# Optimization experiments

Hardware: AMD Instinct MI355X
Metric: run time of the kernel (lower is better)

The kernel has to match this reference:

```python
import jax, jax.numpy as jnp
import numpy as np

B, T, I, H = 512, 256, 256, 512


def _lstm(x, Wih, Whh, bih, bhh):
    # x: [B, T, I]; Wih: [4H, I]; Whh: [4H, H]; gate order i, f, g, o (torch)
    Bv = x.shape[0]
    Hv = Whh.shape[1]
    xg = jnp.einsum('bti,gi->btg', x, Wih) + bih + bhh  # [B, T, 4H] (input projections hoisted out of scan)
    xg = jnp.transpose(xg, (1, 0, 2))  # [T, B, 4H]
    h0 = jnp.zeros((Bv, Hv), x.dtype)
    c0 = jnp.zeros((Bv, Hv), x.dtype)

    def step(carry, gx):
        h, c = carry
        g = gx + h @ Whh.T  # [B, 4H]
        i, f, gg, o = jnp.split(g, 4, axis=-1)
        i = jax.nn.sigmoid(i)
        f = jax.nn.sigmoid(f)
        gg = jnp.tanh(gg)
        o = jax.nn.sigmoid(o)
        c = f * c + i * gg
        h = o * jnp.tanh(c)
        return (h, c), h

    _, hs = jax.lax.scan(step, (h0, c0), xg)  # hs: [T, B, H]
    return jnp.transpose(hs, (1, 0, 2))  # [B, T, H]


def _bn1d(x, gamma, beta, eps=1e-5):
    # torch BatchNorm1d on [N, C, L] in training mode: per-channel stats over (N, L), biased var
    m = jnp.mean(x, axis=(0, 2), keepdims=True)
    v = jnp.var(x, axis=(0, 2), keepdims=True)
    return (x - m) * jax.lax.rsqrt(v + eps) * gamma[None, :, None] + beta[None, :, None]


def setup_inputs() -> dict:
    key = jax.random.key(0)
    ks = jax.random.split(key, 14)
    s = 1.0 / np.sqrt(H)
    return {
        'x': jax.random.normal(ks[0], (B, T, I), jnp.float32),
        'Wih': jax.random.uniform(ks[1], (4 * H, I), jnp.float32, -s, s),
        'Whh': jax.random.uniform(ks[2], (4 * H, H), jnp.float32, -s, s),
        'bih': jax.random.uniform(ks[3], (4 * H,), jnp.float32, -s, s),
        'bhh': jax.random.uniform(ks[4], (4 * H,), jnp.float32, -s, s),
        'fc1_w': jax.random.uniform(ks[5], (32, H), jnp.float32, -s, s),
        'fc1_b': jax.random.uniform(ks[6], (32,), jnp.float32, -s, s),
        'fc2_w': jax.random.uniform(ks[7], (1, 32), jnp.float32, -0.17, 0.17),
        'fc2_b': jax.random.uniform(ks[8], (1,), jnp.float32, -0.17, 0.17),
        'bn1_g': jnp.ones((T,), jnp.float32),
        'bn1_b': jnp.zeros((T,), jnp.float32),
        'bn2_g': jnp.ones((T,), jnp.float32),
        'bn2_b': jnp.zeros((T,), jnp.float32),
    }


def reference(x, Wih, Whh, bih, bhh, fc1_w, fc1_b, fc2_w, fc2_b, bn1_g, bn1_b, bn2_g, bn2_b):
    lstm_out = _lstm(x, Wih, Whh, bih, bhh)  # [B, T, H]
    a = jnp.einsum('bth,oh->bto', lstm_out, fc1_w) + fc1_b  # [B, T, 32]
    a = jax.nn.leaky_relu(_bn1d(a, bn1_g, bn1_b), negative_slope=0.1)
    z = jnp.einsum('bto,po->btp', a, fc2_w) + fc2_b  # [B, T, 1]
    out = jax.nn.relu(_bn1d(z, bn2_g, bn2_b))
    return out
```

## Files before the change

kernel.cpp:

```cpp
#include <hip/hip_runtime.h>

#define BB 512
#define TT 256
#define II 256
#define HH 512

typedef __attribute__((ext_vector_type(8))) short bf16x8;
typedef __attribute__((ext_vector_type(4))) float f32x4;

__device__ __forceinline__ unsigned short f2bf(float f) {
  union { float f; unsigned u; } v; v.f = f;
  unsigned r = v.u + 0x7fffu + ((v.u >> 16) & 1u);
  return (unsigned short)(r >> 16);
}

#define OFF_CNT   0
#define OFF_HSWZ  4096
#define OFF_XSWZ  1052672ULL
#define OFF_HIST  68161536ULL
#define ZERO_WORDS 263168

__global__ void zero_k(unsigned* __restrict__ p, int n) {
  int i = blockIdx.x * blockDim.x + threadIdx.x;
  if (i < n) p[i] = 0u;
}

__global__ __launch_bounds__(256) void prep_x(const float* __restrict__ x,
                                              unsigned char* __restrict__ ws) {
  __shared__ unsigned short xs[16][264];
  const int t = blockIdx.x >> 5, rc = blockIdx.x & 31;
  const int tid = threadIdx.x;
  {
    const int r = tid >> 4, seg = tid & 15;
    const float* src = x + ((size_t)(rc * 16 + r) * TT + t) * II + seg * 16;
    const float4* s4 = (const float4*)src;
#pragma unroll
    for (int q = 0; q < 4; ++q) {
      float4 v = s4[q];
      xs[r][seg * 16 + q * 4 + 0] = f2bf(v.x);
      xs[r][seg * 16 + q * 4 + 1] = f2bf(v.y);
      xs[r][seg * 16 + q * 4 + 2] = f2bf(v.z);
      xs[r][seg * 16 + q * 4 + 3] = f2bf(v.w);
    }
  }
  __syncthreads();
  const int lane = tid & 63;
  const int row16 = lane & 15, koff = (lane >> 4) * 8;
#pragma unroll
  for (int kc = tid >> 6; kc < 8; kc += 4) {
    union { unsigned short h[8]; uint4 v; } pk;
#pragma unroll
    for (int j = 0; j < 8; ++j) pk.h[j] = xs[row16][kc * 32 + koff + j];
    *(uint4*)(ws + OFF_XSWZ + (size_t)(t * 8 + kc) * 32768u +
              ((size_t)rc * 64 + lane) * 16) = pk.v;
  }
}

__global__ __launch_bounds__(512, 2) void lstm_persist(
    const float* __restrict__ Wih, const float* __restrict__ Whh,
    const float* __restrict__ bih, const float* __restrict__ bhh,
    unsigned char* __restrict__ ws)
{
  const int gid = blockIdx.x;
  const int group = gid & 7;
  const int m = gid >> 3;
  const int tid = threadIdx.x;
  const int wv = tid >> 6, lane = tid & 63;
  const int mb = wv & 3, kh = wv >> 2;
  const int lq = lane >> 4, ln = lane & 15;

  int* flags_g = (int*)(ws + OFF_CNT + (size_t)group * 512);
  unsigned char* xswz  = ws + OFF_XSWZ;
  unsigned char* hswz0 = ws + OFF_HSWZ;
  unsigned char* hswz1 = ws + OFF_HSWZ + 524288;
  unsigned char* hist  = ws + OFF_HIST;

  __shared__ int step_flag;
  if (tid == 0) step_flag = 0;

  bf16x8 Wf[12][4];
#pragma unroll
  for (int kk = 0; kk < 12; ++kk) {
    const int kb = (kh * 12 + kk) * 32 + lq * 8;
#pragma unroll
    for (int nt = 0; nt < 4; ++nt) {
      const int gcol = nt * 512 + m * 16 + ln;
      const float* s = (kb < 256) ? (Wih + (size_t)gcol * 256 + kb)
                                  : (Whh + (size_t)gcol * 512 + (kb - 256));
      bf16x8 w;
#pragma unroll
      for (int j = 0; j < 8; ++j) w[j] = (short)f2bf(s[j]);
      Wf[kk][nt] = w;
    }
  }

  float bia[4];
#pragma unroll
  for (int nt = 0; nt < 4; ++nt) {
    int gcol = nt * 512 + m * 16 + ln;
    bia[nt] = bih[gcol] + bhh[gcol];
  }

  __shared__ float g_s[64 * 68];
  __shared__ float h_s[64 * 17];

  const size_t aoff = ((size_t)(group * 4 + mb) * 64 + lane) * 16;
  float creg[4] = {0.f, 0.f, 0.f, 0.f};
  const f32x4 zero4 = {0.f, 0.f, 0.f, 0.f};

#pragma unroll 1
  for (int t = 0; t < 256; ++t) {
    unsigned char* hrd = (t & 1) ? hswz1 : hswz0;
    unsigned char* hwr = (t & 1) ? hswz0 : hswz1;

    f32x4 acc[4] = {zero4, zero4, zero4, zero4};

    if (kh == 0) {
#pragma unroll
      for (int kk = 0; kk < 8; ++kk) {
        bf16x8 a = *(const bf16x8*)(xswz + (size_t)(t * 8 + kk) * 32768u + aoff);
#pragma unroll
        for (int nt = 0; nt < 4; ++nt)
          acc[nt] = __builtin_amdgcn_mfma_f32_16x16x32_bf16(a, Wf[kk][nt], acc[nt], 0, 0, 0);
      }
    }

    if (t > 0) {
      if (wv == 4) {
        int iter = 0;
        for (;;) {
          int v = __hip_atomic_load(flags_g + (lane & 31), __ATOMIC_RELAXED,
                                    __HIP_MEMORY_SCOPE_AGENT);
          if (__all(v >= t)) break;
          if (++iter >= (1 << 17)) break;
          __builtin_amdgcn_s_sleep(1);
        }
        __hip_atomic_store(&step_flag, t, __ATOMIC_RELAXED,
                           __HIP_MEMORY_SCOPE_WORKGROUP);
      } else {
        int iter = 0;
        while (__hip_atomic_load(&step_flag, __ATOMIC_RELAXED,
                                 __HIP_MEMORY_SCOPE_WORKGROUP) < t
               && iter < (1 << 20)) {
          ++iter;
          __builtin_amdgcn_s_sleep(1);
        }
      }
      asm volatile("" ::: "memory");
    }

    if (kh == 0) {
      unsigned long long u0[4], u1[4];
#pragma unroll
      for (int p = 0; p < 4; ++p) {
        const unsigned long long* q =
            (const unsigned long long*)(hrd + (size_t)p * 32768u + aoff);
        u0[p] = __hip_atomic_load(q + 0, __ATOMIC_RELAXED, __HIP_MEMORY_SCOPE_AGENT);
        u1[p] = __hip_atomic_load(q + 1, __ATOMIC_RELAXED, __HIP_MEMORY_SCOPE_AGENT);
      }
#pragma unroll
      for (int kk = 0; kk < 4; ++kk) {
        union { unsigned long long q[2]; bf16x8 v; } u;
        u.q[0] = u0[kk]; u.q[1] = u1[kk];
#pragma unroll
        for (int nt = 0; nt < 4; ++nt)
          acc[nt] = __builtin_amdgcn_mfma_f32_16x16x32_bf16(u.v, Wf[8 + kk][nt], acc[nt], 0, 0, 0);
      }
    } else {
      unsigned long long u0[6], u1[6];
#pragma unroll
      for (int p = 0; p < 6; ++p) {
        const unsigned long long* q =
            (const unsigned long long*)(hrd + (size_t)(4 + p) * 32768u + aoff);
        u0[p] = __hip_atomic_load(q + 0, __ATOMIC_RELAXED, __HIP_MEMORY_SCOPE_AGENT);
        u1[p] = __hip_atomic_load(q + 1, __ATOMIC_RELAXED, __HIP_MEMORY_SCOPE_AGENT);
      }
#pragma unroll
      for (int kk = 0; kk < 12; ++kk) {
        const int slot = kk % 6;
        union { unsigned long long q[2]; bf16x8 v; } u;
        u.q[0] = u0[slot]; u.q[1] = u1[slot];
        if (kk < 6) {
          const unsigned long long* q =
              (const unsigned long long*)(hrd + (size_t)(10 + kk) * 32768u + aoff);
          u0[slot] = __hip_atomic_load(q + 0, __ATOMIC_RELAXED, __HIP_MEMORY_SCOPE_AGENT);
          u1[slot] = __hip_atomic_load(q + 1, __ATOMIC_RELAXED, __HIP_MEMORY_SCOPE_AGENT);
        }
#pragma unroll
        for (int nt = 0; nt < 4; ++nt)
          acc[nt] = __builtin_amdgcn_mfma_f32_16x16x32_bf16(u.v, Wf[kk][nt], acc[nt], 0, 0, 0);
      }
#pragma unroll
      for (int nt = 0; nt < 4; ++nt)
#pragma unroll
        for (int r = 0; r < 4; ++r)
          g_s[(mb * 16 + lq * 4 + r) * 68 + nt * 16 + ln] = acc[nt][r];
    }
    __syncthreads();

    if (kh == 0) {
#pragma unroll
      for (int r = 0; r < 4; ++r) {
        const int rw = mb * 16 + lq * 4 + r;
        float gi = acc[0][r] + g_s[rw * 68 + ln]      + bia[0];
        float gf = acc[1][r] + g_s[rw * 68 + 16 + ln] + bia[1];
        float gg = acc[2][r] + g_s[rw * 68 + 32 + ln] + bia[2];
        float go = acc[3][r] + g_s[rw * 68 + 48 + ln] + bia[3];
        float iv = 1.f / (1.f + __expf(-gi));
        float fv = 1.f / (1.f + __expf(-gf));
        float gv = 1.f - 2.f / (__expf(2.f * gg) + 1.f);
        float ov = 1.f / (1.f + __expf(-go));
        float cv = fv * creg[r] + iv * gv;
        creg[r] = cv;
        h_s[rw * 17 + ln] = ov * (1.f - 2.f / (__expf(2.f * cv) + 1.f));
      }
    }
    __syncthreads();

    if (tid < 128) {
      int rc_l = tid >> 5;
      int lane_off = tid & 31;
      int l2 = (m & 1) * 32 + lane_off;
      int rowl = rc_l * 16 + (lane_off & 15);
      int jb = (lane_off >> 4) * 8;
      union { unsigned short s[8]; uint4 v; } pk;
#pragma unroll
      for (int j = 0; j < 8; ++j) pk.s[j] = f2bf(h_s[rowl * 17 + jb + j]);
      size_t off = ((size_t)((m >> 1) * 32 + group * 4 + rc_l) * 64 + l2) * 16;
      *(uint4*)(hwr + off) = pk.v;
    }
    __syncthreads();

    if (tid == 0)
      __hip_atomic_store(flags_g + m, t + 1, __ATOMIC_RELAXED,
                         __HIP_MEMORY_SCOPE_AGENT);

    if (tid < 128) {
      int row = tid >> 1, jb = (tid & 1) * 8;
      union { unsigned short s[8]; uint4 v; } hq;
#pragma unroll
      for (int j = 0; j < 8; ++j) hq.s[j] = f2bf(h_s[row * 17 + jb + j]);
      int b = group * 64 + row;
      *(uint4*)(hist + ((size_t)(b * 256 + t) * 512 + m * 16 + jb) * 2) = hq.v;
    }
  }
}

__global__ __launch_bounds__(256) void e1_fc1(
    const float* __restrict__ fc1_w, const unsigned char* __restrict__ hist,
    float* __restrict__ a_out)
{
  const int tid = threadIdx.x, wv = tid >> 6, lane = tid & 63;
  const int lq = lane >> 4, ln = lane & 15;

  bf16x8 Bf[16][2];
#pragma unroll
  for (int kk = 0; kk < 16; ++kk) {
#pragma unroll
    for (int nt = 0; nt < 2; ++nt) {
      const float* s = fc1_w + (size_t)(nt * 16 + ln) * 512 + kk * 32 + lq * 8;
      bf16x8 w;
#pragma unroll
      for (int j = 0; j < 8; ++j) w[j] = (short)f2bf(s[j]);
      Bf[kk][nt] = w;
    }
  }

  const int rbase = blockIdx.x * 128 + wv * 32;
  const f32x4 zero4 = {0.f, 0.f, 0.f, 0.f};
  f32x4 acc[2][2] = {{zero4, zero4}, {zero4, zero4}};
#pragma unroll
  for (int kk = 0; kk < 16; ++kk) {
    bf16x8 a0 = *(const bf16x8*)(hist + ((size_t)(rbase + ln) * 512 + kk * 32 + lq * 8) * 2);
    bf16x8 a1 = *(const bf16x8*)(hist + ((size_t)(rbase + 16 + ln) * 512 + kk * 32 + lq * 8) * 2);
#pragma unroll
    for (int nt = 0; nt < 2; ++nt) {
      acc[0][nt] = __builtin_amdgcn_mfma_f32_16x16x32_bf16(a0, Bf[kk][nt], acc[0][nt], 0, 0, 0);
      acc[1][nt] = __builtin_amdgcn_mfma_f32_16x16x32_bf16(a1, Bf[kk][nt], acc[1][nt], 0, 0, 0);
    }
  }
#pragma unroll
  for (int mt = 0; mt < 2; ++mt)
#pragma unroll
    for (int nt = 0; nt < 2; ++nt)
#pragma unroll
      for (int r = 0; r < 4; ++r) {
        int row = rbase + mt * 16 + lq * 4 + r;
        a_out[(size_t)row * 32 + nt * 16 + ln] = acc[mt][nt][r];
      }
}

__global__ __launch_bounds__(256) void e2_head(
    const float* __restrict__ a_in, const float* __restrict__ fc1_b,
    const float* __restrict__ fc2_w, const float* __restrict__ fc2_b,
    const float* __restrict__ bn1_g, const float* __restrict__ bn1_b,
    const float* __restrict__ bn2_g, const float* __restrict__ bn2_b,
    float* __restrict__ out)
{
  const int t = blockIdx.x, tid = threadIdx.x;
  __shared__ float fb[32], fw[32];
  __shared__ float red[4][2], red2[4][2];
  if (tid < 32) { fb[tid] = fc1_b[tid]; fw[tid] = fc2_w[tid]; }
  __syncthreads();

  float va[2][32];
  float s1 = 0.f, s2 = 0.f;
#pragma unroll
  for (int rr = 0; rr < 2; ++rr) {
    int b = tid * 2 + rr;
    const float* p = a_in + ((size_t)b * 256 + t) * 32;
#pragma unroll
    for (int o = 0; o < 32; ++o) {
      float v = p[o] + fb[o];
      va[rr][o] = v;
      s1 += v; s2 += v * v;
    }
  }
#pragma unroll
  for (int off = 32; off > 0; off >>= 1) {
    s1 += __shfl_down(s1, off);
    s2 += __shfl_down(s2, off);
  }
  if ((tid & 63) == 0) { red[tid >> 6][0] = s1; red[tid >> 6][1] = s2; }
  __syncthreads();
  float tot1 = red[0][0] + red[1][0] + red[2][0] + red[3][0];
  float tot2 = red[0][1] + red[1][1] + red[2][1] + red[3][1];
  float m1 = tot1 * (1.f / 16384.f);
  float v1 = tot2 * (1.f / 16384.f) - m1 * m1;
  float sc1 = bn1_g[t] * rsqrtf(v1 + 1e-5f);
  float sh1 = bn1_b[t];

  float z[2];
  float zs1 = 0.f, zs2 = 0.f;
#pragma unroll
  for (int rr = 0; rr < 2; ++rr) {
    float acc = fc2_b[0];
#pragma unroll
    for (int o = 0; o < 32; ++o) {
      float av = (va[rr][o] - m1) * sc1 + sh1;
      av = (av > 0.f) ? av : 0.1f * av;
      acc += av * fw[o];
    }
    z[rr] = acc; zs1 += acc; zs2 += acc * acc;
  }
#pragma unroll
  for (int off = 32; off > 0; off >>= 1) {
    zs1 += __shfl_down(zs1, off);
    zs2 += __shfl_down(zs2, off);
  }
  if ((tid & 63) == 0) { red2[tid >> 6][0] = zs1; red2[tid >> 6][1] = zs2; }
  __syncthreads();
  float zt1 = red2[0][0] + red2[1][0] + red2[2][0] + red2[3][0];
  float zt2 = red2[0][1] + red2[1][1] + red2[2][1] + red2[3][1];
  float m2 = zt1 * (1.f / 512.f);
  float v2 = zt2 * (1.f / 512.f) - m2 * m2;
  float sc2 = bn2_g[t] * rsqrtf(v2 + 1e-5f);
  float sh2 = bn2_b[t];
#pragma unroll
  for (int rr = 0; rr < 2; ++rr) {
    int b = tid * 2 + rr;
    float res = (z[rr] - m2) * sc2 + sh2;
    out[(size_t)b * 256 + t] = (res > 0.f) ? res : 0.f;
  }
}

extern "C" void kernel_launch(void* const* d_in, const int* in_sizes, int n_in,
                              void* d_out, int out_size, void* d_ws, size_t ws_size,
                              hipStream_t stream) {
  const float* x    = (const float*)d_in[0];
  const float* Wih  = (const float*)d_in[1];
  const float* Whh  = (const float*)d_in[2];
  const float* bih  = (const float*)d_in[3];
  const float* bhh  = (const float*)d_in[4];
  const float* fc1w = (const float*)d_in[5];
  const float* fc1b = (const float*)d_in[6];
  const float* fc2w = (const float*)d_in[7];
  const float* fc2b = (const float*)d_in[8];
  const float* b1g  = (const float*)d_in[9];
  const float* b1b  = (const float*)d_in[10];
  const float* b2g  = (const float*)d_in[11];
  const float* b2b  = (const float*)d_in[12];
  unsigned char* ws = (unsigned char*)d_ws;
  float* out = (float*)d_out;
  float* a_buf = (float*)(ws + OFF_XSWZ);

  zero_k<<<1028, 256, 0, stream>>>((unsigned*)ws, ZERO_WORDS);
  prep_x<<<8192, 256, 0, stream>>>(x, ws);
  lstm_persist<<<256, 512, 0, stream>>>(Wih, Whh, bih, bhh, ws);
  e1_fc1<<<1024, 256, 0, stream>>>(fc1w, ws + OFF_HIST, a_buf);
  e2_head<<<256, 256, 0, stream>>>(a_buf, fc1b, fc2w, fc2b, b1g, b1b, b2g, b2b, out);
}
```

Before: 1.461 ms.

## Repartition LSTM persistent blocks into 32 batch groups of 16 rows

Changes the work split of the persistent LSTM kernel from 8 batch groups × 32 hidden slices to 32 batch groups of 16 rows × 8 hidden slices of 64 units. Each wave now owns one gate and four 16-column subtiles, the block stages the shared h tile into LDS once instead of every wave loading it from global memory, and the cell update is spread over all threads. Each block now waits on only 8 peer flags instead of 32, which is meant to cut synchronisation latency per timestep. The cost is an extra LDS staging pass, an extra barrier, and a larger shared-memory footprint.

After: 1.484 ms. Within noise of the previous version (+1.6%).

```diff
diff --git a/kernel.cpp b/kernel.cpp
--- a/kernel.cpp
+++ b/kernel.cpp
@@ -62,14 +62,14 @@
     unsigned char* __restrict__ ws)
 {
   const int gid = blockIdx.x;
-  const int group = gid & 7;
-  const int m = gid >> 3;
+  const int g = gid & 31;
+  const int m = gid >> 5;
   const int tid = threadIdx.x;
   const int wv = tid >> 6, lane = tid & 63;
-  const int mb = wv & 3, kh = wv >> 2;
+  const int nh = wv & 3, kh = wv >> 2;
   const int lq = lane >> 4, ln = lane & 15;
 
-  int* flags_g = (int*)(ws + OFF_CNT + (size_t)group * 512);
+  int* flags_g = (int*)(ws + (size_t)g * 128);
   unsigned char* xswz  = ws + OFF_XSWZ;
   unsigned char* hswz0 = ws + OFF_HSWZ;
   unsigned char* hswz1 = ws + OFF_HSWZ + 524288;
@@ -83,29 +83,33 @@
   for (int kk = 0; kk < 12; ++kk) {
     const int kb = (kh * 12 + kk) * 32 + lq * 8;
 #pragma unroll
-    for (int nt = 0; nt < 4; ++nt) {
-      const int gcol = nt * 512 + m * 16 + ln;
+    for (int ns = 0; ns < 4; ++ns) {
+      const int gcol = nh * 512 + m * 64 + ns * 16 + ln;
       const float* s = (kb < 256) ? (Wih + (size_t)gcol * 256 + kb)
                                   : (Whh + (size_t)gcol * 512 + (kb - 256));
       bf16x8 w;
 #pragma unroll
       for (int j = 0; j < 8; ++j) w[j] = (short)f2bf(s[j]);
-      Wf[kk][nt] = w;
-    }
-  }
-
-  float bia[4];
-#pragma unroll
-  for (int nt = 0; nt < 4; ++nt) {
-    int gcol = nt * 512 + m * 16 + ln;
-    bia[nt] = bih[gcol] + bhh[gcol];
-  }
-
-  __shared__ float g_s[64 * 68];
-  __shared__ float h_s[64 * 17];
-
-  const size_t aoff = ((size_t)(group * 4 + mb) * 64 + lane) * 16;
-  float creg[4] = {0.f, 0.f, 0.f, 0.f};
+      Wf[kk][ns] = w;
+    }
+  }
+
+  const int urow = tid >> 5;
+  const int ujl  = (tid & 31) * 2;
+  float bia2[2][4];
+#pragma unroll
+  for (int cc = 0; cc < 2; ++cc)
+#pragma unroll
+    for (int nt = 0; nt < 4; ++nt) {
+      int gcol = nt * 512 + m * 64 + ujl + cc;
+      bia2[cc][nt] = bih[gcol] + bhh[gcol];
+    }
+
+  __shared__ float g_s[8704];
+  __shared__ float h_s[1088];
+  __shared__ unsigned long long hstage[2048];
+
+  float c2[2] = {0.f, 0.f};
   const f32x4 zero4 = {0.f, 0.f, 0.f, 0.f};
 
 #pragma unroll 1
@@ -117,11 +121,12 @@
 
     if (kh == 0) {
 #pragma unroll
-      for (int kk = 0; kk < 8; ++kk) {
-        bf16x8 a = *(const bf16x8*)(xswz + (size_t)(t * 8 + kk) * 32768u + aoff);
-#pragma unroll
-        for (int nt = 0; nt < 4; ++nt)
-          acc[nt] = __builtin_amdgcn_mfma_f32_16x16x32_bf16(a, Wf[kk][nt], acc[nt], 0, 0, 0);
+      for (int kc = 0; kc < 8; ++kc) {
+        bf16x8 a = *(const bf16x8*)(xswz + (size_t)(t * 8 + kc) * 32768u +
+                                    ((size_t)(g * 64 + lane)) * 16);
+#pragma unroll
+        for (int ns = 0; ns < 4; ++ns)
+          acc[ns] = __builtin_amdgcn_mfma_f32_16x16x32_bf16(a, Wf[kc][ns], acc[ns], 0, 0, 0);
       }
     }
 
@@ -129,7 +134,7 @@
       if (wv == 4) {
         int iter = 0;
         for (;;) {
-          int v = __hip_atomic_load(flags_g + (lane & 31), __ATOMIC_RELAXED,
+          int v = __hip_atomic_load(flags_g + (lane & 7), __ATOMIC_RELAXED,
                                     __HIP_MEMORY_SCOPE_AGENT);
           if (__all(v >= t)) break;
           if (++iter >= (1 << 17)) break;
@@ -149,85 +154,79 @@
       asm volatile("" ::: "memory");
     }
 
+    {
+#pragma unroll
+      for (int i = 0; i < 2; ++i) {
+        const int p = (tid >> 6) + i * 8;
+        const unsigned long long* src = (const unsigned long long*)
+            (hrd + (size_t)p * 32768u + (size_t)g * 1024u + (size_t)lane * 16u);
+        unsigned long long q0 = __hip_atomic_load(src + 0, __ATOMIC_RELAXED,
+                                                  __HIP_MEMORY_SCOPE_AGENT);
+        unsigned long long q1 = __hip_atomic_load(src + 1, __ATOMIC_RELAXED,
+                                                  __HIP_MEMORY_SCOPE_AGENT);
+        hstage[tid * 2 + i * 1024] = q0;
+        hstage[tid * 2 + i * 1024 + 1] = q1;
+      }
+    }
+    __syncthreads();
+
+    const unsigned char* hs = (const unsigned char*)hstage;
     if (kh == 0) {
-      unsigned long long u0[4], u1[4];
 #pragma unroll
       for (int p = 0; p < 4; ++p) {
-        const unsigned long long* q =
-            (const unsigned long long*)(hrd + (size_t)p * 32768u + aoff);
-        u0[p] = __hip_atomic_load(q + 0, __ATOMIC_RELAXED, __HIP_MEMORY_SCOPE_AGENT);
-        u1[p] = __hip_atomic_load(q + 1, __ATOMIC_RELAXED, __HIP_MEMORY_SCOPE_AGENT);
-      }
-#pragma unroll
-      for (int kk = 0; kk < 4; ++kk) {
-        union { unsigned long long q[2]; bf16x8 v; } u;
-        u.q[0] = u0[kk]; u.q[1] = u1[kk];
-#pragma unroll
-        for (int nt = 0; nt < 4; ++nt)
-          acc[nt] = __builtin_amdgcn_mfma_f32_16x16x32_bf16(u.v, Wf[8 + kk][nt], acc[nt], 0, 0, 0);
+        bf16x8 a = *(const bf16x8*)(hs + p * 1024 + lane * 16);
+#pragma unroll
+        for (int ns = 0; ns < 4; ++ns)
+          acc[ns] = __builtin_amdgcn_mfma_f32_16x16x32_bf16(a, Wf[8 + p][ns], acc[ns], 0, 0, 0);
       }
     } else {
-      unsigned long long u0[6], u1[6];
-#pragma unroll
-      for (int p = 0; p < 6; ++p) {
-        const unsigned long long* q =
-            (const unsigned long long*)(hrd + (size_t)(4 + p) * 32768u + aoff);
-        u0[p] = __hip_atomic_load(q + 0, __ATOMIC_RELAXED, __HIP_MEMORY_SCOPE_AGENT);
-        u1[p] = __hip_atomic_load(q + 1, __ATOMIC_RELAXED, __HIP_MEMORY_SCOPE_AGENT);
-      }
 #pragma unroll
       for (int kk = 0; kk < 12; ++kk) {
-        const int slot = kk % 6;
-        union { unsigned long long q[2]; bf16x8 v; } u;
-        u.q[0] = u0[slot]; u.q[1] = u1[slot];
-        if (kk < 6) {
-          const unsigned long long* q =
-              (const unsigned long long*)(hrd + (size_t)(10 + kk) * 32768u + aoff);
-          u0[slot] = __hip_atomic_load(q + 0, __ATOMIC_RELAXED, __HIP_MEMORY_SCOPE_AGENT);
-          u1[slot] = __hip_atomic_load(q + 1, __ATOMIC_RELAXED, __HIP_MEMORY_SCOPE_AGENT);
-        }
-#pragma unroll
-        for (int nt = 0; nt < 4; ++nt)
-          acc[nt] = __builtin_amdgcn_mfma_f32_16x16x32_bf16(u.v, Wf[kk][nt], acc[nt], 0, 0, 0);
-      }
-#pragma unroll
-      for (int nt = 0; nt < 4; ++nt)
-#pragma unroll
-        for (int r = 0; r < 4; ++r)
-          g_s[(mb * 16 + lq * 4 + r) * 68 + nt * 16 + ln] = acc[nt][r];
-    }
+        bf16x8 a = *(const bf16x8*)(hs + (4 + kk) * 1024 + lane * 16);
+#pragma unroll
+        for (int ns = 0; ns < 4; ++ns)
+          acc[ns] = __builtin_amdgcn_mfma_f32_16x16x32_bf16(a, Wf[kk][ns], acc[ns], 0, 0, 0);
+      }
+    }
+#pragma unroll
+    for (int ns = 0; ns < 4; ++ns)
+#pragma unroll
+      for (int r = 0; r < 4; ++r)
+        g_s[((kh * 16 + lq * 4 + r) * 4 + nh) * 68 + ns * 16 + ln] = acc[ns][r];
     __syncthreads();
 
-    if (kh == 0) {
-#pragma unroll
-      for (int r = 0; r < 4; ++r) {
-        const int rw = mb * 16 + lq * 4 + r;
-        float gi = acc[0][r] + g_s[rw * 68 + ln]      + bia[0];
-        float gf = acc[1][r] + g_s[rw * 68 + 16 + ln] + bia[1];
-        float gg = acc[2][r] + g_s[rw * 68 + 32 + ln] + bia[2];
-        float go = acc[3][r] + g_s[rw * 68 + 48 + ln] + bia[3];
+    {
+#pragma unroll
+      for (int cc = 0; cc < 2; ++cc) {
+        const int jl = ujl + cc;
+        float gi = g_s[((0 * 16 + urow) * 4 + 0) * 68 + jl]
+                 + g_s[((1 * 16 + urow) * 4 + 0) * 68 + jl] + bia2[cc][0];
+        float gf = g_s[((0 * 16 + urow) * 4 + 1) * 68 + jl]
+                 + g_s[((1 * 16 + urow) * 4 + 1) * 68 + jl] + bia2[cc][1];
+        float gg = g_s[((0 * 16 + urow) * 4 + 2) * 68 + jl]
+                 + g_s[((1 * 16 + urow) * 4 + 2) * 68 + jl] + bia2[cc][2];
+        float go = g_s[((0 * 16 + urow) * 4 + 3) * 68 + jl]
+                 + g_s[((1 * 16 + urow) * 4 + 3) * 68 + jl] + bia2[cc][3];
         float iv = 1.f / (1.f + __expf(-gi));
         float fv = 1.f / (1.f + __expf(-gf));
         float gv = 1.f - 2.f / (__expf(2.f * gg) + 1.f);
         float ov = 1.f / (1.f + __expf(-go));
-        float cv = fv * creg[r] + iv * gv;
-        creg[r] = cv;
-        h_s[rw * 17 + ln] = ov * (1.f - 2.f / (__expf(2.f * cv) + 1.f));
+        float cv = fv * c2[cc] + iv * gv;
+        c2[cc] = cv;
+        h_s[urow * 68 + jl] = ov * (1.f - 2.f / (__expf(2.f * cv) + 1.f));
       }
     }
     __syncthreads();
 
     if (tid < 128) {
-      int rc_l = tid >> 5;
-      int lane_off = tid & 31;
-      int l2 = (m & 1) * 32 + lane_off;
-      int rowl = rc_l * 16 + (lane_off & 15);
-      int jb = (lane_off >> 4) * 8;
+      int cc = tid >> 6;
+      int lp = tid & 63;
       union { unsigned short s[8]; uint4 v; } pk;
 #pragma unroll
-      for (int j = 0; j < 8; ++j) pk.s[j] = f2bf(h_s[rowl * 17 + jb + j]);
-      size_t off = ((size_t)((m >> 1) * 32 + group * 4 + rc_l) * 64 + l2) * 16;
-      *(uint4*)(hwr + off) = pk.v;
+      for (int j = 0; j < 8; ++j)
+        pk.s[j] = f2bf(h_s[(lp & 15) * 68 + cc * 32 + (lp >> 4) * 8 + j]);
+      *(uint4*)(hwr + (size_t)(2 * m + cc) * 32768u + (size_t)g * 1024u +
+                (size_t)lp * 16u) = pk.v;
     }
     __syncthreads();
 
@@ -236,12 +235,12 @@
                          __HIP_MEMORY_SCOPE_AGENT);
 
     if (tid < 128) {
-      int row = tid >> 1, jb = (tid & 1) * 8;
+      int row = tid >> 3, jl0 = (tid & 7) * 8;
       union { unsigned short s[8]; uint4 v; } hq;
 #pragma unroll
-      for (int j = 0; j < 8; ++j) hq.s[j] = f2bf(h_s[row * 17 + jb + j]);
-      int b = group * 64 + row;
-      *(uint4*)(hist + ((size_t)(b * 256 + t) * 512 + m * 16 + jb) * 2) = hq.v;
+      for (int j = 0; j < 8; ++j) hq.s[j] = f2bf(h_s[row * 68 + jl0 + j]);
+      int b = g * 16 + row;
+      *(uint4*)(hist + ((size_t)(b * 256 + t) * 512 + m * 64 + jl0) * 2) = hq.v;
     }
   }
 }
```
